# Optimization experiments

Hardware: AMD Instinct MI355X
Metric: run time of the kernel (lower is better)

Reference implementation:

```python
import jax, jax.numpy as jnp
import numpy as np

D_MODEL = 512
NHEAD = 8
WINDOW = 64


def setup_inputs() -> dict:
    key = jax.random.key(0)
    ks = jax.random.split(key, 5)
    d = D_MODEL
    x = jax.random.normal(ks[0], (8, 2048, d), dtype=jnp.float32)
    # nn.MultiheadAttention params: packed in-proj [3d, d] + bias [3d], out-proj [d, d] + bias [d]
    scale = 1.0 / np.sqrt(d)
    in_proj_w = jax.random.normal(ks[1], (3 * d, d), dtype=jnp.float32) * scale
    in_proj_b = jnp.zeros((3 * d,), dtype=jnp.float32)
    out_proj_w = jax.random.normal(ks[2], (d, d), dtype=jnp.float32) * scale
    out_proj_b = jnp.zeros((d,), dtype=jnp.float32)
    return {"x": x, "in_proj_w": in_proj_w, "in_proj_b": in_proj_b,
            "out_proj_w": out_proj_w, "out_proj_b": out_proj_b}


def reference(x, in_proj_w, in_proj_b, out_proj_w, out_proj_b):
    B, L, d = x.shape
    H = NHEAD
    dh = d // H
    # packed qkv projection (torch Linear: x @ W.T + b)
    qkv = jnp.einsum('bld,ed->ble', x, in_proj_w) + in_proj_b  # [B, L, 3d]
    q, k, v = jnp.split(qkv, 3, axis=-1)
    # split heads -> [B, H, L, dh]
    def heads(t):
        return t.reshape(B, L, H, dh).transpose(0, 2, 1, 3)
    q, k, v = heads(q), heads(k), heads(v)
    scores = jnp.einsum('bhqd,bhkd->bhqk', q, k) / jnp.sqrt(jnp.float32(dh))
    # banded mask: positions with |i-j| > window are masked out
    idx = jnp.arange(L)
    band = jnp.abs(idx[None, :] - idx[:, None]) > WINDOW  # [L, L] bool
    scores = jnp.where(band[None, None, :, :], jnp.float32(-jnp.inf), scores)
    p = jax.nn.softmax(scores, axis=-1)
    out = jnp.einsum('bhqk,bhkd->bhqd', p, v)  # [B, H, L, dh]
    out = out.transpose(0, 2, 1, 3).reshape(B, L, d)
    return jnp.einsum('bld,ed->ble', out, out_proj_w) + out_proj_b
```

## Files before the change

### kernel.cpp

```cpp
#include <hip/hip_runtime.h>

typedef __bf16 bf16x8 __attribute__((ext_vector_type(8)));
typedef unsigned short u16;
typedef unsigned short u16x8 __attribute__((ext_vector_type(8)));
typedef float f32x4 __attribute__((ext_vector_type(4)));

#define L_SEQ 2048
#define NQT   (L_SEQ / 128)

__device__ __forceinline__ float bf2f(u16 x) {
    unsigned u = ((unsigned)x) << 16;
    return __builtin_bit_cast(float, u);
}
__device__ __forceinline__ u16 f2bf(float f) {
    unsigned u = __builtin_bit_cast(unsigned, f);
    u += 0x7FFFu + ((u >> 16) & 1u);
    return (u16)(u >> 16);
}

__device__ __forceinline__ void gload_lds16(const u16* g, u16* l) {
    __builtin_amdgcn_global_load_lds(
        (const __attribute__((address_space(1))) void*)g,
        (__attribute__((address_space(3))) void*)l, 16, 0, 0);
}

__global__ void cvt_f32_bf16(const float* __restrict__ in, u16* __restrict__ out, int n8) {
    const int i = blockIdx.x * blockDim.x + threadIdx.x;
    if (i >= n8) return;
    const float4* p = reinterpret_cast<const float4*>(in) + (size_t)i * 2;
    const float4 a = p[0], b = p[1];
    u16x8 r;
    r[0] = f2bf(a.x); r[1] = f2bf(a.y); r[2] = f2bf(a.z); r[3] = f2bf(a.w);
    r[4] = f2bf(b.x); r[5] = f2bf(b.y); r[6] = f2bf(b.z); r[7] = f2bf(b.w);
    *(reinterpret_cast<u16x8*>(out) + i) = r;
}

template <bool OUT_BF16>
__launch_bounds__(256)
__global__ void gemm_bt_bias(const u16* __restrict__ A, const u16* __restrict__ W,
                             const float* __restrict__ bias, void* __restrict__ Cv,
                             int M, int N, int K) {
    __shared__ u16 As[128 * 32];
    __shared__ u16 Bs[128 * 32];

    const int tid   = threadIdx.x;
    const int lane  = tid & 63;
    const int wid   = tid >> 6;
    const int wm    = wid >> 1;
    const int wn    = wid & 1;
    const int row_l = lane & 15;
    const int grp   = lane >> 4;

    const int m0 = blockIdx.y * 128;
    const int n0 = blockIdx.x * 128;

    const int st_row = tid >> 2;
    const int st_col = (tid & 3) * 8;
    const u16* gA = A + (size_t)(m0 + st_row) * K + st_col;
    const u16* gB = W + (size_t)(n0 + st_row) * K + st_col;
    u16* lA = As + wid * 512;
    u16* lB = Bs + wid * 512;

    f32x4 acc[4][4];
#pragma unroll
    for (int mi = 0; mi < 4; ++mi)
#pragma unroll
        for (int ni = 0; ni < 4; ++ni)
            acc[mi][ni] = (f32x4){0.f, 0.f, 0.f, 0.f};

    for (int k0 = 0; k0 < K; k0 += 32) {
#pragma unroll
        for (int i = 0; i < 2; ++i) {
            gload_lds16(gA + (size_t)i * 64 * K + k0, lA + i * 2048);
            gload_lds16(gB + (size_t)i * 64 * K + k0, lB + i * 2048);
        }
        __syncthreads();

        bf16x8 a[4], b[4];
#pragma unroll
        for (int mi = 0; mi < 4; ++mi)
            a[mi] = *reinterpret_cast<const bf16x8*>(&As[(wm * 64 + mi * 16 + row_l) * 32 + grp * 8]);
#pragma unroll
        for (int ni = 0; ni < 4; ++ni)
            b[ni] = *reinterpret_cast<const bf16x8*>(&Bs[(wn * 64 + ni * 16 + row_l) * 32 + grp * 8]);
#pragma unroll
        for (int mi = 0; mi < 4; ++mi)
#pragma unroll
            for (int ni = 0; ni < 4; ++ni)
                acc[mi][ni] = __builtin_amdgcn_mfma_f32_16x16x32_bf16(a[mi], b[ni], acc[mi][ni], 0, 0, 0);
        __syncthreads();
    }

#pragma unroll
    for (int ni = 0; ni < 4; ++ni) {
        const int col = n0 + wn * 64 + ni * 16 + row_l;
        const float bsf = bias[col];
#pragma unroll
        for (int mi = 0; mi < 4; ++mi) {
#pragma unroll
            for (int r = 0; r < 4; ++r) {
                const int rowm = m0 + wm * 64 + mi * 16 + grp * 4 + r;
                const float v = acc[mi][ni][r] + bsf;
                if (OUT_BF16)
                    ((u16*)Cv)[(size_t)rowm * N + col] = f2bf(v);
                else
                    ((float*)Cv)[(size_t)rowm * N + col] = v;
            }
        }
    }
}

__launch_bounds__(512, 4)
__global__ void local_attn(const u16* __restrict__ qkv, u16* __restrict__ att) {
    __shared__ __align__(16) u16 Ks[256 * 64];
    __shared__ __align__(16) u16 Vt[64 * 256];
    __shared__ __align__(16) u16 Pl[8][512];

    const int tid   = threadIdx.x;
    const int lane  = tid & 63;
    const int wv    = tid >> 6;
    const int row_l = lane & 15;
    const int grp   = lane >> 4;
    const int qt = blockIdx.x, h = blockIdx.y, b = blockIdx.z;
    const int q0b = qt * 128;
    const int kstart = q0b - 64;
    const size_t base = (size_t)b * L_SEQ * 1536;
    const bool edge = (qt == 0) || (qt == NQT - 1);

    {
        const int r0 = tid >> 3;
        const int c  = tid & 7;
#pragma unroll
        for (int i = 0; i < 4; ++i) {
            const int row  = i * 64 + r0;
            const int keyg = min(max(kstart + row, 0), L_SEQ - 1);
            const int cg   = c ^ (row & 7);
            gload_lds16(qkv + base + (size_t)keyg * 1536 + 512 + h * 64 + cg * 8,
                        &Ks[i * 4096 + wv * 512]);
        }
    }
    {
#pragma unroll
        for (int i = 0; i < 4; ++i) {
            const int idx  = i * 512 + tid;
            const int row  = idx >> 3;
            const int c8   = idx & 7;
            const int keyg = min(max(kstart + row, 0), L_SEQ - 1);
            const u16x8 vu = *reinterpret_cast<const u16x8*>(
                qkv + base + (size_t)keyg * 1536 + 1024 + h * 64 + c8 * 8);
#pragma unroll
            for (int e = 0; e < 8; ++e) {
                const int d = c8 * 8 + e;
                Vt[d * 256 + (((row >> 3) ^ (d & 7)) * 8) + (row & 7)] = vu[e];
            }
        }
    }

    const int qrow_g = q0b + wv * 16 + row_l;
    const u16* qp = qkv + base + (size_t)qrow_g * 1536 + h * 64;
    const bf16x8 qf0 = *reinterpret_cast<const bf16x8*>(qp + grp * 8);
    const bf16x8 qf1 = *reinterpret_cast<const bf16x8*>(qp + 32 + grp * 8);

    __syncthreads();

    float m_r = -1e30f, l_r = 0.f;
    f32x4 acc[4];
#pragma unroll
    for (int ds = 0; ds < 4; ++ds) acc[ds] = (f32x4){0.f, 0.f, 0.f, 0.f};
    u16* Pw = Pl[wv];

    auto do_chunk = [&](int c, bool bandLo, bool bandHi, bool half, bool rng) {
        const int kcL = wv * 16 + 32 * c;
        const int kcG = kstart + kcL;
        const int nf = half ? 1 : 2;

        f32x4 s[2];
#pragma unroll
        for (int f = 0; f < 2; ++f) {
            if (f >= nf) break;
            const int rr = kcL + 16 * f + row_l;
            const bf16x8 ka = *reinterpret_cast<const bf16x8*>(
                &Ks[rr * 64 + ((grp ^ (rr & 7)) * 8)]);
            const bf16x8 kb = *reinterpret_cast<const bf16x8*>(
                &Ks[rr * 64 + (((grp + 4) ^ (rr & 7)) * 8)]);
            f32x4 z = (f32x4){0.f, 0.f, 0.f, 0.f};
            z = __builtin_amdgcn_mfma_f32_16x16x32_bf16(ka, qf0, z, 0, 0, 0);
            z = __builtin_amdgcn_mfma_f32_16x16x32_bf16(kb, qf1, z, 0, 0, 0);
            s[f] = z;
        }

        float p[2][4];
        float cmax = -1e30f;
#pragma unroll
        for (int f = 0; f < 2; ++f) {
            if (f >= nf) break;
#pragma unroll
            for (int r = 0; r < 4; ++r) {
                const int k = 16 * f + grp * 4 + r;
                bool ok = true;
                if (bandLo) ok = ok && (k >= row_l);
                if (bandHi) ok = ok && (k <= row_l);
                if (rng) { const int kg = kcG + k; ok = ok && (kg >= 0) && (kg < L_SEQ); }
                const float sv = ok ? s[f][r] * 0.125f : -1e30f;
                p[f][r] = sv;
                cmax = fmaxf(cmax, sv);
            }
        }
        cmax = fmaxf(cmax, __shfl_xor(cmax, 16, 64));
        cmax = fmaxf(cmax, __shfl_xor(cmax, 32, 64));
        const float mn  = fmaxf(m_r, cmax);
        const float scl = __expf(m_r - mn);
        m_r = mn;
        float lsum = 0.f;
#pragma unroll
        for (int f = 0; f < 2; ++f) {
            if (f >= nf) break;
#pragma unroll
            for (int r = 0; r < 4; ++r) {
                const float pv = (p[f][r] <= -1e29f) ? 0.f : __expf(p[f][r] - mn);
                p[f][r] = pv;
                lsum += pv;
            }
        }
        lsum += __shfl_xor(lsum, 16, 64);
        lsum += __shfl_xor(lsum, 32, 64);
        l_r = l_r * scl + lsum;

        float scl4[4];
#pragma unroll
        for (int r = 0; r < 4; ++r) scl4[r] = __shfl(scl, grp * 4 + r, 64);
#pragma unroll
        for (int ds = 0; ds < 4; ++ds)
#pragma unroll
            for (int r = 0; r < 4; ++r) acc[ds][r] *= scl4[r];

#pragma unroll
        for (int f = 0; f < 2; ++f)
#pragma unroll
            for (int r = 0; r < 4; ++r) {
                const int k = 16 * f + grp * 4 + r;
                const int slot = (k >> 3) ^ ((row_l >> 1) & 3);
                const float pv = (f < nf) ? p[f][r] : 0.f;
                Pw[row_l * 32 + slot * 8 + (k & 7)] = f2bf(pv);
            }
        const bf16x8 pa = *reinterpret_cast<const bf16x8*>(
            &Pw[row_l * 32 + ((grp ^ ((row_l >> 1) & 3)) * 8)]);

        int k0 = kcL + grp * 8;
        if (half) k0 = min(k0, 248);
#pragma unroll
        for (int ds = 0; ds < 4; ++ds) {
            const int d = ds * 16 + row_l;
            const bf16x8 vf = *reinterpret_cast<const bf16x8*>(
                &Vt[d * 256 + (((k0 >> 3) ^ (d & 7)) * 8)]);
            acc[ds] = __builtin_amdgcn_mfma_f32_16x16x32_bf16(pa, vf, acc[ds], 0, 0, 0);
        }
    };

    if (!edge) {
        do_chunk(0, true,  false, false, false);
        do_chunk(1, false, false, false, false);
        do_chunk(2, false, false, false, false);
        do_chunk(3, false, false, false, false);
        do_chunk(4, false, true,  true,  false);
    } else {
        const int kw = kstart + wv * 16;
        if (kw       > -32 && kw       < L_SEQ) do_chunk(0, true,  false, false, true);
        if (kw + 32  > -32 && kw + 32  < L_SEQ) do_chunk(1, false, false, false, true);
        if (kw + 64  > -32 && kw + 64  < L_SEQ) do_chunk(2, false, false, false, true);
        if (kw + 96  > -32 && kw + 96  < L_SEQ) do_chunk(3, false, false, false, true);
        if (kw + 128 > -32 && kw + 128 < L_SEQ) do_chunk(4, false, true,  true,  true);
    }

    const float inv = 1.f / l_r;
    float inv4[4];
#pragma unroll
    for (int r = 0; r < 4; ++r) inv4[r] = __shfl(inv, grp * 4 + r, 64);
    const int qg = q0b + wv * 16 + grp * 4;
#pragma unroll
    for (int r = 0; r < 4; ++r)
#pragma unroll
        for (int ds = 0; ds < 4; ++ds)
            att[(size_t)(b * L_SEQ + qg + r) * 512 + h * 64 + ds * 16 + row_l] =
                f2bf(acc[ds][r] * inv4[r]);
}

extern "C" void kernel_launch(void* const* d_in, const int* in_sizes, int n_in,
                              void* d_out, int out_size, void* d_ws, size_t ws_size,
                              hipStream_t stream) {
    const float* x     = (const float*)d_in[0];
    const float* w_in  = (const float*)d_in[1];
    const float* b_in  = (const float*)d_in[2];
    const float* w_out = (const float*)d_in[3];
    const float* b_out = (const float*)d_in[4];
    float* out = (float*)d_out;

    const int B = 8, L = L_SEQ;
    const int M = B * L;

    u16* qkv   = (u16*)d_ws;
    u16* att   = qkv   + (size_t)M * 1536;
    u16* x_bf  = att   + (size_t)M * 512;
    u16* wi_bf = x_bf  + (size_t)M * 512;
    u16* wo_bf = wi_bf + (size_t)1536 * 512;

    {
        const int nx = M * 512 / 8;
        cvt_f32_bf16<<<(nx + 255) / 256, 256, 0, stream>>>(x, x_bf, nx);
        const int nwi = 1536 * 512 / 8;
        cvt_f32_bf16<<<(nwi + 255) / 256, 256, 0, stream>>>(w_in, wi_bf, nwi);
        const int nwo = 512 * 512 / 8;
        cvt_f32_bf16<<<(nwo + 255) / 256, 256, 0, stream>>>(w_out, wo_bf, nwo);
    }

    gemm_bt_bias<true><<<dim3(1536 / 128, M / 128), dim3(256), 0, stream>>>(
        x_bf, wi_bf, b_in, qkv, M, 1536, 512);

    local_attn<<<dim3(NQT, 8, B), dim3(512), 0, stream>>>(qkv, att);

    gemm_bt_bias<false><<<dim3(512 / 128, M / 128), dim3(256), 0, stream>>>(
        att, wo_bf, b_out, out, M, 512, 512);
}
```

Baseline: 104.0 us.

## Double-buffer GEMM LDS tiles with BK=64, XOR swizzle and tile remap

Reworks the projection GEMM mainloop. The K-tile grows from 32 to 64, and two LDS buffers let the next tile's global-to-LDS loads be issued while the current tile is computed, with one barrier per iteration. Column chunks are XOR-swizzled by row to avoid LDS bank conflicts, and workgroup IDs are remapped in groups of 8, presumably to spread tiles across XCDs for cache locality. LDS use grows to 64KB per block, which may lower occupancy. The code also assumes K is a multiple of 64 and the tile count is divisible by 8.

Result: faster. 95.51 us (-8.1%).

```diff
diff --git a/kernel.cpp b/kernel.cpp
--- a/kernel.cpp
+++ b/kernel.cpp
@@ -40,8 +40,8 @@
 __global__ void gemm_bt_bias(const u16* __restrict__ A, const u16* __restrict__ W,
                              const float* __restrict__ bias, void* __restrict__ Cv,
                              int M, int N, int K) {
-    __shared__ u16 As[128 * 32];
-    __shared__ u16 Bs[128 * 32];
+    __shared__ u16 As[2][128 * 64];
+    __shared__ u16 Bs[2][128 * 64];
 
     const int tid   = threadIdx.x;
     const int lane  = tid & 63;
@@ -51,15 +51,16 @@
     const int row_l = lane & 15;
     const int grp   = lane >> 4;
 
-    const int m0 = blockIdx.y * 128;
-    const int n0 = blockIdx.x * 128;
-
-    const int st_row = tid >> 2;
-    const int st_col = (tid & 3) * 8;
-    const u16* gA = A + (size_t)(m0 + st_row) * K + st_col;
-    const u16* gB = W + (size_t)(n0 + st_row) * K + st_col;
-    u16* lA = As + wid * 512;
-    u16* lB = Bs + wid * 512;
+    const int nwg  = gridDim.x * gridDim.y;
+    const int hw   = blockIdx.y * gridDim.x + blockIdx.x;
+    const int tile = (hw & 7) * (nwg >> 3) + (hw >> 3);
+    const int m0 = (tile / gridDim.x) * 128;
+    const int n0 = (tile % gridDim.x) * 128;
+
+    const int srow = tid >> 3;
+    const int scol = ((tid & 7) ^ (srow & 7)) * 8;
+    const u16* gA = A + (size_t)(m0 + srow) * K + scol;
+    const u16* gB = W + (size_t)(n0 + srow) * K + scol;
 
     f32x4 acc[4][4];
 #pragma unroll
@@ -68,28 +69,48 @@
         for (int ni = 0; ni < 4; ++ni)
             acc[mi][ni] = (f32x4){0.f, 0.f, 0.f, 0.f};
 
-    for (int k0 = 0; k0 < K; k0 += 32) {
-#pragma unroll
-        for (int i = 0; i < 2; ++i) {
-            gload_lds16(gA + (size_t)i * 64 * K + k0, lA + i * 2048);
-            gload_lds16(gB + (size_t)i * 64 * K + k0, lB + i * 2048);
-        }
+    auto stage = [&](int buf, int kt) {
+#pragma unroll
+        for (int i = 0; i < 4; ++i) {
+            gload_lds16(gA + (size_t)(i * 32) * K + kt * 64, &As[buf][i * 2048 + wid * 512]);
+            gload_lds16(gB + (size_t)(i * 32) * K + kt * 64, &Bs[buf][i * 2048 + wid * 512]);
+        }
+    };
+
+    auto compute = [&](int buf) {
+#pragma unroll
+        for (int kk = 0; kk < 2; ++kk) {
+            bf16x8 a[4], b[4];
+#pragma unroll
+            for (int mi = 0; mi < 4; ++mi) {
+                const int row = wm * 64 + mi * 16 + row_l;
+                a[mi] = *reinterpret_cast<const bf16x8*>(
+                    &As[buf][row * 64 + (((kk * 4 + grp) ^ (row & 7)) * 8)]);
+            }
+#pragma unroll
+            for (int ni = 0; ni < 4; ++ni) {
+                const int row = wn * 64 + ni * 16 + row_l;
+                b[ni] = *reinterpret_cast<const bf16x8*>(
+                    &Bs[buf][row * 64 + (((kk * 4 + grp) ^ (row & 7)) * 8)]);
+            }
+#pragma unroll
+            for (int mi = 0; mi < 4; ++mi)
+#pragma unroll
+                for (int ni = 0; ni < 4; ++ni)
+                    acc[mi][ni] = __builtin_amdgcn_mfma_f32_16x16x32_bf16(a[mi], b[ni], acc[mi][ni], 0, 0, 0);
+        }
+    };
+
+    const int NT = K >> 6;
+    stage(0, 0);
+    __syncthreads();
+    for (int t = 0; t < NT - 1; ++t) {
+        const int cur = t & 1;
+        stage(cur ^ 1, t + 1);
+        compute(cur);
         __syncthreads();
-
-        bf16x8 a[4], b[4];
-#pragma unroll
-        for (int mi = 0; mi < 4; ++mi)
-            a[mi] = *reinterpret_cast<const bf16x8*>(&As[(wm * 64 + mi * 16 + row_l) * 32 + grp * 8]);
-#pragma unroll
-        for (int ni = 0; ni < 4; ++ni)
-            b[ni] = *reinterpret_cast<const bf16x8*>(&Bs[(wn * 64 + ni * 16 + row_l) * 32 + grp * 8]);
-#pragma unroll
-        for (int mi = 0; mi < 4; ++mi)
-#pragma unroll
-            for (int ni = 0; ni < 4; ++ni)
-                acc[mi][ni] = __builtin_amdgcn_mfma_f32_16x16x32_bf16(a[mi], b[ni], acc[mi][ni], 0, 0, 0);
-        __syncthreads();
-    }
+    }
+    compute((NT - 1) & 1);
 
 #pragma unroll
     for (int ni = 0; ni < 4; ++ni) {
```
